# Performance work log

Measured on AMD Instinct MI355X. Metric: run time of the kernel, lower is better.

The kernel has to match this reference:

```python
import jax, jax.numpy as jnp
import numpy as np

B, N, S = 32, 1000, 200
D, H, DK, FF, NL = 128, 8, 16, 512, 3
HK = H * DK


def _mha(x, Wq, Wk, Wv, Wo, bo):
    # x: [B, L, D]; manual multi-head attention matching the torch code
    Bv, L, _ = x.shape
    q = (x @ Wq).reshape(Bv, L, H, DK).transpose(0, 2, 1, 3)  # [B,H,L,dk]
    k = (x @ Wk).reshape(Bv, L, H, DK).transpose(0, 2, 1, 3)
    v = (x @ Wv).reshape(Bv, L, H, DK).transpose(0, 2, 1, 3)
    score = jnp.einsum('bhid,bhjd->bhij', q, k) / jnp.sqrt(jnp.asarray(DK, x.dtype))
    w = jax.nn.softmax(score, axis=-1)
    o = jnp.einsum('bhij,bhjd->bhid', w, v).transpose(0, 2, 1, 3).reshape(Bv, L, HK)
    return o @ Wo + bo


def _decoder_layer(x, Wq, Wk, Wv, Wo, bo, W1, b1, W2, b2):
    out1 = x + _mha(x, Wq, Wk, Wv, Wo, bo)
    ff = jax.nn.relu(out1 @ W1 + b1) @ W2 + b2
    return out1 + ff


def _forward(data, attention_bias, Wfirst, bfirst, Wlast, blast,
             Wq, Wk, Wv, Wo, bo, W1, b1, W2, b2, Wfin, bfin, sel):
    Bv, Np, Dm = data.shape
    Sn = sel.shape[1]
    bidx = jnp.arange(Bv)
    # _get_new_data: ordered list of unselected node indices, shape [B, N-S]
    mask = jnp.zeros((Bv, Np), bool).at[bidx[:, None], sel].set(True)
    vals = jnp.where(mask, Np, jnp.arange(Np)[None, :])
    unselect = jnp.sort(vals, axis=1)[:, : Np - Sn]            # [B, N-S]
    left = jnp.take_along_axis(data, unselect[:, :, None], axis=1)  # [B, N-S, D]
    # _get_encoding for first / last selected node
    first = data[bidx, sel[:, 0]]
    last = data[bidx, sel[:, -1]]
    ef = first @ Wfirst + bfirst
    el = last @ Wlast + blast
    out = jnp.concatenate([ef[:, None], left, el[:, None]], axis=1)  # [B, N-S+2, D]
    for i in range(Wq.shape[0]):
        out = _decoder_layer(out, Wq[i], Wk[i], Wv[i], Wo[i], bo[i],
                             W1[i], b1[i], W2[i], b2[i])
    logits = (out @ Wfin + bfin)[..., 0]                       # [B, N-S+2]
    # attention bias of current (last selected) node, gathered at unselected
    ab_cur = attention_bias[bidx, sel[:, -1]]                  # [B, N]
    ab_uns = jnp.take_along_axis(ab_cur, unselect, axis=1)     # [B, N-S]
    logits = logits.at[:, 1:-1].add(ab_uns)
    L = logits.shape[1]
    pos = jnp.arange(L)
    end_mask = (pos == 0) | (pos == L - 1)
    logits = jnp.where(end_mask[None, :], -jnp.inf, logits)
    props = jax.nn.softmax(logits, axis=-1)[:, 1:-1]           # [B, N-S]
    props = jnp.where(props <= 1e-5, props + 1e-7, props)
    # scatter back: selected positions -> -2, unselected -> props
    new_props = jnp.full((Bv, Np), -2.0, dtype=data.dtype)
    new_props = new_props.at[bidx[:, None], unselect].set(props)
    return new_props


def setup_inputs() -> dict:
    key = jax.random.key(0)
    ks = jax.random.split(key, 24)
    data = jax.random.normal(ks[0], (B, N, D), jnp.float32)
    # selected_node_list must contain unique indices per row (partial tour)
    sel = jax.vmap(lambda k: jax.random.permutation(k, N))(
        jax.random.split(ks[1], B))[:, :S].astype(jnp.int32)
    attention_bias = jax.random.normal(ks[2], (B, N, N), jnp.float32)

    def lin(k, shape, fan_in):
        return jax.random.normal(k, shape, jnp.float32) / np.float32(np.sqrt(fan_in))

    return dict(
        data=data,
        attention_bias=attention_bias,
        Wfirst=lin(ks[3], (D, D), D), bfirst=jnp.zeros((D,), jnp.float32),
        Wlast=lin(ks[4], (D, D), D), blast=jnp.zeros((D,), jnp.float32),
        Wq=lin(ks[5], (NL, D, HK), D),
        Wk=lin(ks[6], (NL, D, HK), D),
        Wv=lin(ks[7], (NL, D, HK), D),
        Wo=lin(ks[8], (NL, HK, D), HK), bo=jnp.zeros((NL, D), jnp.float32),
        W1=lin(ks[9], (NL, D, FF), D), b1=jnp.zeros((NL, FF), jnp.float32),
        W2=lin(ks[10], (NL, FF, D), FF), b2=jnp.zeros((NL, D), jnp.float32),
        Wfin=lin(ks[11], (D, 1), D), bfin=jnp.zeros((1,), jnp.float32),
        selected_node_list=sel,
    )


def reference(data, attention_bias, Wfirst, bfirst, Wlast, blast,
              Wq, Wk, Wv, Wo, bo, W1, b1, W2, b2, Wfin, bfin,
              selected_node_list):
    return _forward(data, attention_bias, Wfirst, bfirst, Wlast, blast,
                    Wq, Wk, Wv, Wo, bo, W1, b1, W2, b2, Wfin, bfin,
                    selected_node_list)
```

## Files before the change

kernel.cpp:

```cpp
#include <hip/hip_runtime.h>
#include <hip/hip_bf16.h>
#include <math.h>

#define NB 32
#define NN 1000
#define SS 200
#define DD 128
#define HH 8
#define DKK 16
#define FFD 512
#define NLAYER 3
#define LQ 802
#define LPAD 832
#define NPADK (LPAD - LQ)
#define MROWS (NB*LQ)
#define NBLK64 (MROWS/64)
#define NQT 26
#define NQT64 13
#define HSTR 516
#define TSTR 132

typedef __attribute__((ext_vector_type(8))) short short8;
typedef __attribute__((ext_vector_type(4))) short short4v;
typedef __attribute__((ext_vector_type(16))) float f32x16;

static __device__ __forceinline__ unsigned short f2bf(float x) {
  union { float f; unsigned int u; } v; v.f = x;
  unsigned int r = v.u + 0x7fff + ((v.u >> 16) & 1);
  return (unsigned short)(r >> 16);
}

#define WCH 196608
__global__ __launch_bounds__(256) void k_wconv(const float* __restrict__ Wq, const float* __restrict__ Wk,
                       const float* __restrict__ Wv, const float* __restrict__ Wo,
                       const float* __restrict__ W1, const float* __restrict__ W2,
                       unsigned short* __restrict__ WtQKV, unsigned short* __restrict__ Wot,
                       unsigned short* __restrict__ W1t, unsigned short* __restrict__ W2t) {
  int e = blockIdx.x*256 + threadIdx.x;
  if (e >= 3*WCH) return;
  int layer = e / WCH, r = e - layer*WCH;
  if (r < 49152) {
    int n = r >> 7, k = r & 127;
    int sect = n >> 7, nn = n & 127;
    const float* W = (sect == 0) ? Wq : (sect == 1) ? Wk : Wv;
    WtQKV[layer*49152 + r] = f2bf(W[layer*16384 + k*128 + nn]);
  } else if (r < 65536) {
    int r2 = r - 49152;
    int n = r2 >> 7, k = r2 & 127;
    Wot[layer*16384 + r2] = f2bf(Wo[layer*16384 + k*128 + n]);
  } else if (r < 131072) {
    int r2 = r - 65536;
    int n = r2 >> 7, k = r2 & 127;
    W1t[layer*65536 + r2] = f2bf(W1[layer*65536 + k*512 + n]);
  } else {
    int r2 = r - 131072;
    int n = r2 >> 9, k = r2 & 511;
    W2t[layer*65536 + r2] = f2bf(W2[layer*65536 + k*128 + n]);
  }
}

__global__ __launch_bounds__(1024) void k_unselect(const int* __restrict__ sel,
                                                   int* __restrict__ unselect,
                                                   int* __restrict__ pos) {
  int b = blockIdx.x;
  int n = threadIdx.x;
  __shared__ int bufA[1024];
  __shared__ int bufB[1024];
  bufA[n] = (n < NN) ? 1 : 0;
  __syncthreads();
  if (n < SS) bufA[sel[b*SS + n]] = 0;
  __syncthreads();
  int flag = bufA[n];
  int* src = bufA; int* dst = bufB;
  for (int off = 1; off < 1024; off <<= 1) {
    int v = src[n];
    if (n >= off) v += src[n - off];
    __syncthreads();
    dst[n] = v;
    __syncthreads();
    int* tp = src; src = dst; dst = tp;
  }
  if (n < NN) {
    if (flag) {
      int j = src[n] - 1;
      unselect[b*800 + j] = n;
      pos[b*NN + n] = j + 1;
    } else {
      pos[b*NN + n] = -1;
    }
  }
}

__global__ __launch_bounds__(128) void k_embed_ends(const float* __restrict__ data,
                       const int* __restrict__ sel,
                       const float* __restrict__ Wfirst, const float* __restrict__ bfirst,
                       const float* __restrict__ Wlast, const float* __restrict__ blast,
                       float* __restrict__ X, unsigned short* __restrict__ Xbf) {
  int which = blockIdx.x, b = blockIdx.y, d = threadIdx.x;
  int l = (which == 0) ? 0 : LQ-1;
  __shared__ float xr[DD];
  int src = sel[b*SS + (which == 0 ? 0 : SS-1)];
  const float* W    = (which == 0) ? Wfirst : Wlast;
  const float* bias = (which == 0) ? bfirst : blast;
  xr[d] = data[((size_t)b*NN + src)*DD + d];
  __syncthreads();
  float acc = bias[d];
  #pragma unroll 4
  for (int k = 0; k < DD; ++k) acc += xr[k] * W[k*DD + d];
  size_t off = ((size_t)(b*LQ + l))*DD + d;
  X[off] = acc;
  Xbf[off] = f2bf(acc);
}

__global__ __launch_bounds__(256) void k_embed_mid(const float* __restrict__ data,
                       const int* __restrict__ unselect,
                       float* __restrict__ X, unsigned short* __restrict__ Xbf) {
  int e = blockIdx.x*256 + threadIdx.x;
  int r = e >> 5;
  int c4 = (e & 31) * 4;
  int b = r / 800, j = r - b*800;
  int nidx = unselect[r];
  const float4 v = *(const float4*)&data[((size_t)b*NN + nidx)*DD + c4];
  size_t off = ((size_t)(b*LQ + 1 + j))*DD + c4;
  *(float4*)&X[off] = v;
  unsigned short p0 = f2bf(v.x), p1 = f2bf(v.y), p2 = f2bf(v.z), p3 = f2bf(v.w);
  ushort4 pk; pk.x = p0; pk.y = p1; pk.z = p2; pk.w = p3;
  *(ushort4*)&Xbf[off] = pk;
}

__global__ __launch_bounds__(256) void k_qkv_mfma(const unsigned short* __restrict__ Xbf,
                       const unsigned short* __restrict__ Wt,
                       unsigned short* __restrict__ Qb, unsigned short* __restrict__ Kb,
                       unsigned short* __restrict__ Vb) {
  int row0 = blockIdx.x * 64;
  int t = threadIdx.x, wave = t >> 6, lane = t & 63;
  int col = lane & 31, half = lane >> 5;
  short8 a[2][8];
  const unsigned short* xb = Xbf + (size_t)(row0 + col)*DD + half*8;
  #pragma unroll
  for (int mi = 0; mi < 2; ++mi)
    #pragma unroll
    for (int s = 0; s < 8; ++s)
      a[mi][s] = *(const short8*)(xb + (size_t)mi*32*DD + s*16);
  #pragma unroll
  for (int nn = 0; nn < 3; ++nn) {
    int ni = wave*3 + nn;
    short8 bfr[8];
    const unsigned short* wb = Wt + (size_t)(ni*32 + col)*DD + half*8;
    #pragma unroll
    for (int s = 0; s < 8; ++s) bfr[s] = *(const short8*)(wb + s*16);
    f32x16 acc0 = {0.f,0.f,0.f,0.f,0.f,0.f,0.f,0.f,0.f,0.f,0.f,0.f,0.f,0.f,0.f,0.f};
    f32x16 acc1 = {0.f,0.f,0.f,0.f,0.f,0.f,0.f,0.f,0.f,0.f,0.f,0.f,0.f,0.f,0.f,0.f};
    #pragma unroll
    for (int s = 0; s < 8; ++s) {
      acc0 = __builtin_amdgcn_mfma_f32_32x32x16_bf16(a[0][s], bfr[s], acc0, 0, 0, 0);
      acc1 = __builtin_amdgcn_mfma_f32_32x32x16_bf16(a[1][s], bfr[s], acc1, 0, 0, 0);
    }
    int n = ni*32 + col;
    int sect = n >> 7, nc = n & 127;
    int h = nc >> 4, d = nc & 15;
    #pragma unroll
    for (int mi = 0; mi < 2; ++mi) {
      const f32x16& acc = mi ? acc1 : acc0;
      #pragma unroll
      for (int r = 0; r < 16; ++r) {
        int m = row0 + mi*32 + (r&3) + 8*(r>>2) + 4*half;
        int b_ = m / LQ, l = m - b_*LQ;
        size_t bh = (size_t)(b_*HH + h);
        float v = acc[r];
        if (sect == 0)      Qb[(bh*LPAD + l)*DKK + d] = f2bf(v * 0.25f);
        else if (sect == 1) Kb[(bh*LPAD + l)*DKK + d] = f2bf(v);
        else                Vb[(bh*LPAD + l)*DKK + d] = f2bf(v);
      }
    }
  }
}

__global__ __launch_bounds__(256) void k_vt(const unsigned short* __restrict__ Vb,
                                            unsigned short* __restrict__ Vt,
                                            unsigned short* __restrict__ Kb) {
  __shared__ unsigned short Lt[16][72];
  int l0 = blockIdx.x * 64;
  int bh = blockIdx.y;
  int t = threadIdx.x;
  int l = t >> 2, d4 = (t & 3) * 4;
  ushort4 v = {0,0,0,0};
  if (l0 + l < LQ) v = *(const ushort4*)&Vb[((size_t)bh*LPAD + l0 + l)*DKK + d4];
  Lt[d4+0][l] = v.x; Lt[d4+1][l] = v.y; Lt[d4+2][l] = v.z; Lt[d4+3][l] = v.w;
  __syncthreads();
  int dk = t >> 4, lq = (t & 15)*4;
  ushort4 o;
  o.x = Lt[dk][lq]; o.y = Lt[dk][lq+1]; o.z = Lt[dk][lq+2]; o.w = Lt[dk][lq+3];
  *(ushort4*)&Vt[((size_t)bh*DKK + dk)*LPAD + l0 + lq] = o;
  if (blockIdx.x == 12 && t < 240)
    ((unsigned int*)&Kb[((size_t)bh*LPAD + LQ)*DKK])[t] = 0u;
}

__global__ __launch_bounds__(256) void k_attn3(const unsigned short* __restrict__ Q,
                       const unsigned short* __restrict__ K,
                       const unsigned short* __restrict__ Vt,
                       unsigned short* __restrict__ Obf) {
  int bid = blockIdx.x;
  int g = bid & 7, i = bid >> 3;
  int bhg = i / NQT64, qt = i - bhg*NQT64;
  int bh = bhg*8 + g;
  int b = bh >> 3, h = bh & 7;
  int q0 = qt*64;
  size_t bhL = (size_t)bh * LPAD;
  int t = threadIdx.x;
  int wave = t >> 6, lane = t & 63;
  int col = lane & 31;
  int half = lane >> 5;
  bool hb = (half != 0);

  __shared__ float mw[2][4][32];
  __shared__ float sw[2][4][32];
  __shared__ float sfin[2][32];
  __shared__ float ored[2][4][16][32];
  __shared__ float osum[2][32][17];

  int q0c = q0 + col;      if (q0c > LQ-1) q0c = LQ-1;
  int q1c = q0 + 32 + col; if (q1c > LQ-1) q1c = LQ-1;
  short8 bQ0 = *(const short8*)&Q[(bhL + q0c)*DKK + half*8];
  short8 bQ1 = *(const short8*)&Q[(bhL + q1c)*DKK + half*8];

  f32x16 oacc0 = {0.f,0.f,0.f,0.f,0.f,0.f,0.f,0.f,0.f,0.f,0.f,0.f,0.f,0.f,0.f,0.f};
  f32x16 oacc1 = oacc0;
  float runm0 = -INFINITY, runs0 = 0.f;
  float runm1 = -INFINITY, runs1 = 0.f;

  for (int kt = wave; kt < NQT; kt += 4) {
    int key0 = kt*32;
    short8 aK = *(const short8*)&K[(bhL + key0 + col)*DKK + half*8];
    short8 aV0 = {0,0,0,0,0,0,0,0};
    short8 aV1 = {0,0,0,0,0,0,0,0};
    if (col < 16) {
      const unsigned short* vp = &Vt[((size_t)bh*DKK + col)*LPAD + key0 + half*8];
      aV0 = *(const short8*)vp;
      aV1 = *(const short8*)(vp + 16);
    }

    auto process = [&](const short8& bQ, f32x16& oacc, float& runm, float& runs) {
      f32x16 c = {0.f,0.f,0.f,0.f,0.f,0.f,0.f,0.f,0.f,0.f,0.f,0.f,0.f,0.f,0.f,0.f};
      c = __builtin_amdgcn_mfma_f32_32x32x16_bf16(aK, bQ, c, 0, 0, 0);
      float tm = c[0];
      #pragma unroll
      for (int r = 1; r < 16; ++r) tm = fmaxf(tm, c[r]);
      tm = fmaxf(tm, __shfl_xor(tm, 32, 64));
      float mnew = fmaxf(runm, tm);
      float scale = __expf(runm - mnew);
      runs *= scale;
      #pragma unroll
      for (int r = 0; r < 8; ++r) oacc[r] *= scale;
      runm = mnew;
      float p[16];
      #pragma unroll
      for (int r = 0; r < 16; ++r) p[r] = __expf(c[r] - mnew);
      float ts = 0.f;
      #pragma unroll
      for (int r = 0; r < 16; ++r) ts += p[r];
      runs += ts;
      unsigned int pk[8];
      #pragma unroll
      for (int j = 0; j < 8; ++j) {
        unsigned int ua = __float_as_uint(p[2*j]);
        unsigned int ub = __float_as_uint(p[2*j+1]);
        pk[j] = (ua >> 16) | (ub & 0xffff0000u);
      }
      int Y0 = __shfl_xor((int)(hb ? pk[0] : pk[2]), 32, 64);
      int Y1 = __shfl_xor((int)(hb ? pk[1] : pk[3]), 32, 64);
      int Y2 = __shfl_xor((int)(hb ? pk[4] : pk[6]), 32, 64);
      int Y3 = __shfl_xor((int)(hb ? pk[5] : pk[7]), 32, 64);
      union { int4 i4; short8 s8; } fA, fB;
      fA.i4.x = hb ? Y0 : (int)pk[0];
      fA.i4.y = hb ? Y1 : (int)pk[1];
      fA.i4.z = hb ? (int)pk[2] : Y0;
      fA.i4.w = hb ? (int)pk[3] : Y1;
      fB.i4.x = hb ? Y2 : (int)pk[4];
      fB.i4.y = hb ? Y3 : (int)pk[5];
      fB.i4.z = hb ? (int)pk[6] : Y2;
      fB.i4.w = hb ? (int)pk[7] : Y3;
      oacc = __builtin_amdgcn_mfma_f32_32x32x16_bf16(aV0, fA.s8, oacc, 0, 0, 0);
      oacc = __builtin_amdgcn_mfma_f32_32x32x16_bf16(aV1, fB.s8, oacc, 0, 0, 0);
    };
    process(bQ0, oacc0, runm0, runs0);
    process(bQ1, oacc1, runm1, runs1);
  }

  float m2v[2], fsv[2];
  #pragma unroll
  for (int u = 0; u < 2; ++u) {
    float runm = u ? runm1 : runm0;
    float runs = u ? runs1 : runs0;
    float pm = __shfl_xor(runm, 32, 64);
    float ps = __shfl_xor(runs, 32, 64);
    float m2 = fmaxf(runm, pm);
    float fself = __expf(runm - m2);
    float s2 = runs*fself + ps*__expf(pm - m2);
    if (half == 0) { mw[u][wave][col] = m2; sw[u][wave][col] = s2; }
    m2v[u] = m2; fsv[u] = fself;
  }
  __syncthreads();
  #pragma unroll
  for (int u = 0; u < 2; ++u) {
    float M = fmaxf(fmaxf(mw[u][0][col], mw[u][1][col]), fmaxf(mw[u][2][col], mw[u][3][col]));
    float S = sw[u][0][col]*__expf(mw[u][0][col]-M) + sw[u][1][col]*__expf(mw[u][1][col]-M)
            + sw[u][2][col]*__expf(mw[u][2][col]-M) + sw[u][3][col]*__expf(mw[u][3][col]-M);
    float fw = __expf(m2v[u] - M) * fsv[u];
    const f32x16& oacc = u ? oacc1 : oacc0;
    #pragma unroll
    for (int r = 0; r < 8; ++r) {
      int dv = (r&3) + 8*(r>>2) + 4*half;
      ored[u][wave][dv][col] = oacc[r] * fw;
    }
    if (wave == 0 && half == 0)
      sfin[u][col] = S - (float)NPADK * __expf(-M);
  }
  __syncthreads();
  {
    int qq = t & 31, dv0 = t >> 5;
    #pragma unroll
    for (int u = 0; u < 2; ++u)
      #pragma unroll
      for (int k = 0; k < 2; ++k) {
        int dv = dv0 + 8*k;
        osum[u][qq][dv] = ored[u][0][dv][qq] + ored[u][1][dv][qq]
                        + ored[u][2][dv][qq] + ored[u][3][dv][qq];
      }
  }
  __syncthreads();
  {
    int qs = t >> 3, c2 = (t & 7)*2;
    #pragma unroll
    for (int u = 0; u < 2; ++u) {
      int q = q0 + u*32 + qs;
      if (q < LQ) {
        float invS = 1.f / sfin[u][qs];
        unsigned int lo = f2bf(osum[u][qs][c2]   * invS);
        unsigned int hi = f2bf(osum[u][qs][c2+1] * invS);
        *(unsigned int*)&Obf[((size_t)(b*LQ + q))*DD + h*DKK + c2] = lo | (hi << 16);
      }
    }
  }
}

__global__ __launch_bounds__(256) void k_pff(const unsigned short* __restrict__ Obf,
        const unsigned short* __restrict__ Wot, const float* __restrict__ bo,
        const unsigned short* __restrict__ W1t, const float* __restrict__ b1,
        const unsigned short* __restrict__ W2t, const float* __restrict__ b2,
        float* __restrict__ X, unsigned short* __restrict__ Xbf) {
  __shared__ __align__(16) unsigned short LDSU[64 * HSTR];
  unsigned short* T  = LDSU;
  unsigned short* Hs = LDSU;
  int row0 = blockIdx.x * 64;
  int t = threadIdx.x, wave = t >> 6, lane = t & 63;
  int col = lane & 31, half = lane >> 5;
  int n = wave*32 + col;
  float res[2][16];
  {
    short8 a[2][8];
    const unsigned short* ob = Obf + (size_t)(row0 + col)*DD + half*8;
    #pragma unroll
    for (int mi = 0; mi < 2; ++mi)
      #pragma unroll
      for (int s = 0; s < 8; ++s)
        a[mi][s] = *(const short8*)(ob + (size_t)mi*32*DD + s*16);
    short8 bfr[8];
    const unsigned short* wb = Wot + (size_t)n*DD + half*8;
    #pragma unroll
    for (int s = 0; s < 8; ++s) bfr[s] = *(const short8*)(wb + s*16);
    f32x16 acc0 = {0.f,0.f,0.f,0.f,0.f,0.f,0.f,0.f,0.f,0.f,0.f,0.f,0.f,0.f,0.f,0.f};
    f32x16 acc1 = acc0;
    #pragma unroll
    for (int s = 0; s < 8; ++s) {
      acc0 = __builtin_amdgcn_mfma_f32_32x32x16_bf16(a[0][s], bfr[s], acc0, 0, 0, 0);
      acc1 = __builtin_amdgcn_mfma_f32_32x32x16_bf16(a[1][s], bfr[s], acc1, 0, 0, 0);
    }
    float bv = bo[n];
    #pragma unroll
    for (int mi = 0; mi < 2; ++mi) {
      const f32x16& acc = mi ? acc1 : acc0;
      #pragma unroll
      for (int r = 0; r < 16; ++r) {
        int ml = mi*32 + (r&3) + 8*(r>>2) + 4*half;
        size_t off = (size_t)(row0 + ml)*DD + n;
        res[mi][r] = X[off] + acc[r] + bv;
        T[ml*TSTR + n] = f2bf(res[mi][r]);
      }
    }
  }
  __syncthreads();
  short8 aF[2][8];
  #pragma unroll
  for (int mi = 0; mi < 2; ++mi)
    #pragma unroll
    for (int s = 0; s < 8; ++s) {
      const unsigned short* tp = &T[(mi*32 + col)*TSTR + half*8 + s*16];
      union { short4v h[2]; short8 v; } u;
      u.h[0] = *(const short4v*)tp;
      u.h[1] = *(const short4v*)(tp + 4);
      aF[mi][s] = u.v;
    }
  __syncthreads();
  #pragma unroll
  for (int nn = 0; nn < 4; ++nn) {
    int ni = wave*4 + nn;
    short8 bfr[8];
    const unsigned short* wb = W1t + (size_t)(ni*32 + col)*DD + half*8;
    #pragma unroll
    for (int s = 0; s < 8; ++s) bfr[s] = *(const short8*)(wb + s*16);
    f32x16 acc0 = {0.f,0.f,0.f,0.f,0.f,0.f,0.f,0.f,0.f,0.f,0.f,0.f,0.f,0.f,0.f,0.f};
    f32x16 acc1 = acc0;
    #pragma unroll
    for (int s = 0; s < 8; ++s) {
      acc0 = __builtin_amdgcn_mfma_f32_32x32x16_bf16(aF[0][s], bfr[s], acc0, 0, 0, 0);
      acc1 = __builtin_amdgcn_mfma_f32_32x32x16_bf16(aF[1][s], bfr[s], acc1, 0, 0, 0);
    }
    int nf = ni*32 + col;
    float bv = b1[nf];
    #pragma unroll
    for (int mi = 0; mi < 2; ++mi) {
      const f32x16& acc = mi ? acc1 : acc0;
      #pragma unroll
      for (int r = 0; r < 16; ++r) {
        int ml = mi*32 + (r&3) + 8*(r>>2) + 4*half;
        Hs[ml*HSTR + nf] = f2bf(fmaxf(acc[r] + bv, 0.f));
      }
    }
  }
  __syncthreads();
  f32x16 acc0 = {0.f,0.f,0.f,0.f,0.f,0.f,0.f,0.f,0.f,0.f,0.f,0.f,0.f,0.f,0.f,0.f};
  f32x16 acc1 = acc0;
  const unsigned short* w2b = W2t + (size_t)n*FFD + half*8;
  #pragma unroll 4
  for (int s = 0; s < 32; ++s) {
    int ko = s*16 + half*8;
    union { short4v h[2]; short8 v; } h0, h1;
    const unsigned short* hp0 = &Hs[col*HSTR + ko];
    const unsigned short* hp1 = &Hs[(32 + col)*HSTR + ko];
    h0.h[0] = *(const short4v*)hp0;  h0.h[1] = *(const short4v*)(hp0 + 4);
    h1.h[0] = *(const short4v*)hp1;  h1.h[1] = *(const short4v*)(hp1 + 4);
    short8 bfr = *(const short8*)(w2b + s*16);
    acc0 = __builtin_amdgcn_mfma_f32_32x32x16_bf16(h0.v, bfr, acc0, 0, 0, 0);
    acc1 = __builtin_amdgcn_mfma_f32_32x32x16_bf16(h1.v, bfr, acc1, 0, 0, 0);
  }
  float bv = b2[n];
  #pragma unroll
  for (int mi = 0; mi < 2; ++mi) {
    const f32x16& acc = mi ? acc1 : acc0;
    #pragma unroll
    for (int r = 0; r < 16; ++r) {
      int ml = mi*32 + (r&3) + 8*(r>>2) + 4*half;
      size_t off = (size_t)(row0 + ml)*DD + n;
      float v = res[mi][r] + acc[r] + bv;
      X[off] = v;
      Xbf[off] = f2bf(v);
    }
  }
}

__global__ __launch_bounds__(256) void k_logits(const float* __restrict__ X,
                        const float* __restrict__ Wfin, const float* __restrict__ bfin,
                        float* __restrict__ logits) {
  int t = threadIdx.x, wave = t >> 6, lane = t & 63;
  int row = blockIdx.x*4 + wave;
  float2 xv = *(const float2*)&X[(size_t)row*DD + lane*2];
  float2 wv = *(const float2*)&Wfin[lane*2];
  float v = xv.x*wv.x + xv.y*wv.y;
  #pragma unroll
  for (int off = 32; off > 0; off >>= 1) v += __shfl_down(v, off);
  if (lane == 0) logits[row] = v + bfin[0];
}

__global__ __launch_bounds__(256) void k_final(const float* __restrict__ logits,
                       const float* __restrict__ AB, const int* __restrict__ sel,
                       const int* __restrict__ unselect, const int* __restrict__ pos,
                       float* __restrict__ out) {
  int b = blockIdx.x, t = threadIdx.x;
  __shared__ float sl[800];
  __shared__ float red[256];
  int lastsel = sel[b*SS + SS-1];
  const float* abrow = AB + ((size_t)b*NN + lastsel)*NN;
  for (int j = t; j < 800; j += 256)
    sl[j] = logits[b*LQ + j + 1] + abrow[unselect[b*800 + j]];
  __syncthreads();
  float lm = -INFINITY;
  for (int j = t; j < 800; j += 256) lm = fmaxf(lm, sl[j]);
  red[t] = lm;
  __syncthreads();
  for (int s = 128; s > 0; s >>= 1) {
    if (t < s) red[t] = fmaxf(red[t], red[t+s]);
    __syncthreads();
  }
  float m = red[0];
  __syncthreads();
  float ls = 0.f;
  for (int j = t; j < 800; j += 256) ls += __expf(sl[j] - m);
  red[t] = ls;
  __syncthreads();
  for (int s = 128; s > 0; s >>= 1) {
    if (t < s) red[t] += red[t+s];
    __syncthreads();
  }
  float inv = 1.f / red[0];
  for (int n = t; n < NN; n += 256) {
    int p1 = pos[b*NN + n];
    float v = -2.0f;
    if (p1 >= 0) {
      float p = __expf(sl[p1-1] - m) * inv;
      if (p <= 1e-5f) p += 1e-7f;
      v = p;
    }
    out[(size_t)b*NN + n] = v;
  }
}

extern "C" void kernel_launch(void* const* d_in, const int* in_sizes, int n_in,
                              void* d_out, int out_size, void* d_ws, size_t ws_size,
                              hipStream_t stream) {
  const float* data   = (const float*)d_in[0];
  const float* AB     = (const float*)d_in[1];
  const float* Wfirst = (const float*)d_in[2];
  const float* bfirst = (const float*)d_in[3];
  const float* Wlast  = (const float*)d_in[4];
  const float* blast  = (const float*)d_in[5];
  const float* Wq     = (const float*)d_in[6];
  const float* Wk     = (const float*)d_in[7];
  const float* Wv     = (const float*)d_in[8];
  const float* Wo     = (const float*)d_in[9];
  const float* bo     = (const float*)d_in[10];
  const float* W1     = (const float*)d_in[11];
  const float* b1     = (const float*)d_in[12];
  const float* W2     = (const float*)d_in[13];
  const float* b2     = (const float*)d_in[14];
  const float* Wfin   = (const float*)d_in[15];
  const float* bfin   = (const float*)d_in[16];
  const int*   sel    = (const int*)d_in[17];
  float* out = (float*)d_out;
  (void)in_sizes; (void)n_in; (void)out_size; (void)ws_size;

  char* ws = (char*)d_ws;
  const size_t NELT = (size_t)MROWS * DD;
  const size_t KVELT = (size_t)NB*HH*LPAD*DKK;
  int*   UNSEL = (int*)ws;
  int*   POS   = (int*)(ws + 102400);
  float* X     = (float*)(ws + 230400);
  unsigned short* Xbf = (unsigned short*)(X + NELT);
  unsigned short* Ob  = Xbf + NELT;
  unsigned short* Qb  = Ob + NELT;
  unsigned short* Kb  = Qb + KVELT;
  unsigned short* Vb  = Kb + KVELT;
  unsigned short* Vt  = Vb + KVELT;
  unsigned short* WtQKV = Vt + KVELT;
  unsigned short* Wot = WtQKV + (size_t)NLAYER*384*128;
  unsigned short* W1t = Wot + (size_t)NLAYER*128*128;
  unsigned short* W2t = W1t + (size_t)NLAYER*512*128;
  float* LOG = (float*)(W2t + (size_t)NLAYER*128*512);

  k_wconv<<<(3*WCH + 255)/256, 256, 0, stream>>>(Wq, Wk, Wv, Wo, W1, W2, WtQKV, Wot, W1t, W2t);
  k_unselect<<<NB, 1024, 0, stream>>>(sel, UNSEL, POS);
  k_embed_ends<<<dim3(2, NB), 128, 0, stream>>>(data, sel, Wfirst, bfirst, Wlast, blast, X, Xbf);
  k_embed_mid<<<3200, 256, 0, stream>>>(data, UNSEL, X, Xbf);
  for (int i = 0; i < NLAYER; ++i) {
    k_qkv_mfma<<<NBLK64, 256, 0, stream>>>(Xbf, WtQKV + (size_t)i*384*128, Qb, Kb, Vb);
    k_vt<<<dim3(13, NB*HH), 256, 0, stream>>>(Vb, Vt, Kb);
    k_attn3<<<NQT64*HH*NB, 256, 0, stream>>>(Qb, Kb, Vt, Ob);
    k_pff<<<NBLK64, 256, 0, stream>>>(Ob, Wot + (size_t)i*128*128, bo + (size_t)i*DD,
                                      W1t + (size_t)i*512*128, b1 + (size_t)i*FFD,
                                      W2t + (size_t)i*128*512, b2 + (size_t)i*DD, X, Xbf);
  }
  k_logits<<<MROWS/4, 256, 0, stream>>>(X, Wfin, bfin, LOG);
  k_final<<<NB, 256, 0, stream>>>(LOG, AB, sel, UNSEL, POS, out);
}
```

Baseline: 557.3 us.

## Restructure attention to one query tile per wave with lazy rescale and exp2

The attention kernel now gives each wave its own 32-query tile and has it walk all key tiles. Before, four waves split the keys and merged partial softmax results through shared memory and several barriers. The query scale folds in log2(e) so exp2 can be used, and the running max is only updated when a tile exceeds it by a threshold. Packed bf16 conversion and max3 instructions replace manual bit tricks. Separately, the unselect prefix sum uses wave ballots instead of a log-step scan, and QKV scatter avoids per-element division; the gains trade fewer waves per block and lazy-rescale numeric risk for removed reductions.

```diff
diff --git a/kernel.cpp b/kernel.cpp
--- a/kernel.cpp
+++ b/kernel.cpp
@@ -16,9 +16,10 @@
 #define MROWS (NB*LQ)
 #define NBLK64 (MROWS/64)
 #define NQT 26
-#define NQT64 13
+#define NQB 7
 #define HSTR 516
 #define TSTR 132
+#define QSCALE 0.3606737602f
 
 typedef __attribute__((ext_vector_type(8))) short short8;
 typedef __attribute__((ext_vector_type(4))) short short4v;
@@ -28,6 +29,18 @@
   union { float f; unsigned int u; } v; v.f = x;
   unsigned int r = v.u + 0x7fff + ((v.u >> 16) & 1);
   return (unsigned short)(r >> 16);
+}
+
+static __device__ __forceinline__ unsigned int cvtpk_bf16(float lo, float hi) {
+  unsigned int r;
+  asm("v_cvt_pk_bf16_f32 %0, %1, %2" : "=v"(r) : "v"(lo), "v"(hi));
+  return r;
+}
+
+static __device__ __forceinline__ float max3f(float a, float b, float c) {
+  float r;
+  asm("v_max3_f32 %0, %1, %2, %3" : "=v"(r) : "v"(a), "v"(b), "v"(c));
+  return r;
 }
 
 #define WCH 196608
@@ -64,25 +77,24 @@
                                                    int* __restrict__ pos) {
   int b = blockIdx.x;
   int n = threadIdx.x;
-  __shared__ int bufA[1024];
-  __shared__ int bufB[1024];
-  bufA[n] = (n < NN) ? 1 : 0;
-  __syncthreads();
-  if (n < SS) bufA[sel[b*SS + n]] = 0;
-  __syncthreads();
-  int flag = bufA[n];
-  int* src = bufA; int* dst = bufB;
-  for (int off = 1; off < 1024; off <<= 1) {
-    int v = src[n];
-    if (n >= off) v += src[n - off];
-    __syncthreads();
-    dst[n] = v;
-    __syncthreads();
-    int* tp = src; src = dst; dst = tp;
-  }
+  __shared__ unsigned char fl[1024];
+  __shared__ int wsum[16];
+  fl[n] = (n < NN) ? 1 : 0;
+  __syncthreads();
+  if (n < SS) fl[sel[b*SS + n]] = 0;
+  __syncthreads();
+  int flag = fl[n];
+  unsigned long long m = __ballot(flag);
+  int lane = n & 63, w = n >> 6;
+  int pre = __popcll(m & ((1ULL << lane) - 1ULL));
+  if (lane == 63) wsum[w] = pre + flag;
+  __syncthreads();
+  int off = 0;
+  #pragma unroll
+  for (int i = 0; i < 16; ++i) off += (i < w) ? wsum[i] : 0;
   if (n < NN) {
     if (flag) {
-      int j = src[n] - 1;
+      int j = off + pre;
       unselect[b*800 + j] = n;
       pos[b*NN + n] = j + 1;
     } else {
@@ -135,6 +147,9 @@
   int row0 = blockIdx.x * 64;
   int t = threadIdx.x, wave = t >> 6, lane = t & 63;
   int col = lane & 31, half = lane >> 5;
+  int b0 = row0 / LQ;
+  int l00 = row0 - b0*LQ;
+  int split = LQ - l00;
   short8 a[2][8];
   const unsigned short* xb = Xbf + (size_t)(row0 + col)*DD + half*8;
   #pragma unroll
@@ -164,11 +179,13 @@
       const f32x16& acc = mi ? acc1 : acc0;
       #pragma unroll
       for (int r = 0; r < 16; ++r) {
-        int m = row0 + mi*32 + (r&3) + 8*(r>>2) + 4*half;
-        int b_ = m / LQ, l = m - b_*LQ;
+        int ml = mi*32 + (r&3) + 8*(r>>2) + 4*half;
+        int over = (ml >= split);
+        int b_ = b0 + over;
+        int l  = over ? (ml - split) : (l00 + ml);
         size_t bh = (size_t)(b_*HH + h);
         float v = acc[r];
-        if (sect == 0)      Qb[(bh*LPAD + l)*DKK + d] = f2bf(v * 0.25f);
+        if (sect == 0)      Qb[(bh*LPAD + l)*DKK + d] = f2bf(v * QSCALE);
         else if (sect == 1) Kb[(bh*LPAD + l)*DKK + d] = f2bf(v);
         else                Vb[(bh*LPAD + l)*DKK + d] = f2bf(v);
       }
@@ -202,34 +219,27 @@
                        unsigned short* __restrict__ Obf) {
   int bid = blockIdx.x;
   int g = bid & 7, i = bid >> 3;
-  int bhg = i / NQT64, qt = i - bhg*NQT64;
+  int bhg = i / NQB, qt = i - bhg*NQB;
   int bh = bhg*8 + g;
   int b = bh >> 3, h = bh & 7;
-  int q0 = qt*64;
   size_t bhL = (size_t)bh * LPAD;
   int t = threadIdx.x;
   int wave = t >> 6, lane = t & 63;
-  int col = lane & 31;
-  int half = lane >> 5;
+  int col = lane & 31, half = lane >> 5;
   bool hb = (half != 0);
 
-  __shared__ float mw[2][4][32];
-  __shared__ float sw[2][4][32];
-  __shared__ float sfin[2][32];
-  __shared__ float ored[2][4][16][32];
-  __shared__ float osum[2][32][17];
-
-  int q0c = q0 + col;      if (q0c > LQ-1) q0c = LQ-1;
-  int q1c = q0 + 32 + col; if (q1c > LQ-1) q1c = LQ-1;
-  short8 bQ0 = *(const short8*)&Q[(bhL + q0c)*DKK + half*8];
-  short8 bQ1 = *(const short8*)&Q[(bhL + q1c)*DKK + half*8];
-
-  f32x16 oacc0 = {0.f,0.f,0.f,0.f,0.f,0.f,0.f,0.f,0.f,0.f,0.f,0.f,0.f,0.f,0.f,0.f};
-  f32x16 oacc1 = oacc0;
-  float runm0 = -INFINITY, runs0 = 0.f;
-  float runm1 = -INFINITY, runs1 = 0.f;
-
-  for (int kt = wave; kt < NQT; kt += 4) {
+  __shared__ __align__(16) unsigned short SO[4][32][20];
+
+  int q0w = qt*128 + wave*32;
+  if (q0w >= LPAD) return;
+
+  int qc = q0w + col; if (qc > LQ-1) qc = LQ-1;
+  short8 bQ = *(const short8*)&Q[(bhL + qc)*DKK + half*8];
+
+  f32x16 oacc = {0.f,0.f,0.f,0.f,0.f,0.f,0.f,0.f,0.f,0.f,0.f,0.f,0.f,0.f,0.f,0.f};
+  float runm = -INFINITY, runs = 0.f;
+
+  for (int kt = 0; kt < NQT; ++kt) {
     int key0 = kt*32;
     short8 aK = *(const short8*)&K[(bhL + key0 + col)*DKK + half*8];
     short8 aV0 = {0,0,0,0,0,0,0,0};
@@ -239,108 +249,74 @@
       aV0 = *(const short8*)vp;
       aV1 = *(const short8*)(vp + 16);
     }
-
-    auto process = [&](const short8& bQ, f32x16& oacc, float& runm, float& runs) {
-      f32x16 c = {0.f,0.f,0.f,0.f,0.f,0.f,0.f,0.f,0.f,0.f,0.f,0.f,0.f,0.f,0.f,0.f};
-      c = __builtin_amdgcn_mfma_f32_32x32x16_bf16(aK, bQ, c, 0, 0, 0);
-      float tm = c[0];
+    f32x16 c = {0.f,0.f,0.f,0.f,0.f,0.f,0.f,0.f,0.f,0.f,0.f,0.f,0.f,0.f,0.f,0.f};
+    c = __builtin_amdgcn_mfma_f32_32x32x16_bf16(aK, bQ, c, 0, 0, 0);
+    float m0 = max3f(c[0],  c[1],  c[2]);
+    float m1 = max3f(c[3],  c[4],  c[5]);
+    float m2 = max3f(c[6],  c[7],  c[8]);
+    float m3 = max3f(c[9],  c[10], c[11]);
+    float m4 = max3f(c[12], c[13], c[14]);
+    float tm = fmaxf(max3f(m0, m1, m2), max3f(m3, m4, c[15]));
+    tm = fmaxf(tm, __shfl_xor(tm, 32, 64));
+    if (!__all(tm <= runm + 11.0f)) {
+      float mnew = fmaxf(runm, tm);
+      float sc = exp2f(runm - mnew);
+      runs *= sc;
       #pragma unroll
-      for (int r = 1; r < 16; ++r) tm = fmaxf(tm, c[r]);
-      tm = fmaxf(tm, __shfl_xor(tm, 32, 64));
-      float mnew = fmaxf(runm, tm);
-      float scale = __expf(runm - mnew);
-      runs *= scale;
-      #pragma unroll
-      for (int r = 0; r < 8; ++r) oacc[r] *= scale;
+      for (int r = 0; r < 8; ++r) oacc[r] *= sc;
       runm = mnew;
-      float p[16];
-      #pragma unroll
-      for (int r = 0; r < 16; ++r) p[r] = __expf(c[r] - mnew);
-      float ts = 0.f;
-      #pragma unroll
-      for (int r = 0; r < 16; ++r) ts += p[r];
-      runs += ts;
-      unsigned int pk[8];
-      #pragma unroll
-      for (int j = 0; j < 8; ++j) {
-        unsigned int ua = __float_as_uint(p[2*j]);
-        unsigned int ub = __float_as_uint(p[2*j+1]);
-        pk[j] = (ua >> 16) | (ub & 0xffff0000u);
-      }
-      int Y0 = __shfl_xor((int)(hb ? pk[0] : pk[2]), 32, 64);
-      int Y1 = __shfl_xor((int)(hb ? pk[1] : pk[3]), 32, 64);
-      int Y2 = __shfl_xor((int)(hb ? pk[4] : pk[6]), 32, 64);
-      int Y3 = __shfl_xor((int)(hb ? pk[5] : pk[7]), 32, 64);
-      union { int4 i4; short8 s8; } fA, fB;
-      fA.i4.x = hb ? Y0 : (int)pk[0];
-      fA.i4.y = hb ? Y1 : (int)pk[1];
-      fA.i4.z = hb ? (int)pk[2] : Y0;
-      fA.i4.w = hb ? (int)pk[3] : Y1;
-      fB.i4.x = hb ? Y2 : (int)pk[4];
-      fB.i4.y = hb ? Y3 : (int)pk[5];
-      fB.i4.z = hb ? (int)pk[6] : Y2;
-      fB.i4.w = hb ? (int)pk[7] : Y3;
-      oacc = __builtin_amdgcn_mfma_f32_32x32x16_bf16(aV0, fA.s8, oacc, 0, 0, 0);
-      oacc = __builtin_amdgcn_mfma_f32_32x32x16_bf16(aV1, fB.s8, oacc, 0, 0, 0);
-    };
-    process(bQ0, oacc0, runm0, runs0);
-    process(bQ1, oacc1, runm1, runs1);
-  }
-
-  float m2v[2], fsv[2];
-  #pragma unroll
-  for (int u = 0; u < 2; ++u) {
-    float runm = u ? runm1 : runm0;
-    float runs = u ? runs1 : runs0;
-    float pm = __shfl_xor(runm, 32, 64);
-    float ps = __shfl_xor(runs, 32, 64);
-    float m2 = fmaxf(runm, pm);
-    float fself = __expf(runm - m2);
-    float s2 = runs*fself + ps*__expf(pm - m2);
-    if (half == 0) { mw[u][wave][col] = m2; sw[u][wave][col] = s2; }
-    m2v[u] = m2; fsv[u] = fself;
-  }
-  __syncthreads();
-  #pragma unroll
-  for (int u = 0; u < 2; ++u) {
-    float M = fmaxf(fmaxf(mw[u][0][col], mw[u][1][col]), fmaxf(mw[u][2][col], mw[u][3][col]));
-    float S = sw[u][0][col]*__expf(mw[u][0][col]-M) + sw[u][1][col]*__expf(mw[u][1][col]-M)
-            + sw[u][2][col]*__expf(mw[u][2][col]-M) + sw[u][3][col]*__expf(mw[u][3][col]-M);
-    float fw = __expf(m2v[u] - M) * fsv[u];
-    const f32x16& oacc = u ? oacc1 : oacc0;
-    #pragma unroll
-    for (int r = 0; r < 8; ++r) {
-      int dv = (r&3) + 8*(r>>2) + 4*half;
-      ored[u][wave][dv][col] = oacc[r] * fw;
-    }
-    if (wave == 0 && half == 0)
-      sfin[u][col] = S - (float)NPADK * __expf(-M);
-  }
-  __syncthreads();
-  {
-    int qq = t & 31, dv0 = t >> 5;
-    #pragma unroll
-    for (int u = 0; u < 2; ++u)
-      #pragma unroll
-      for (int k = 0; k < 2; ++k) {
-        int dv = dv0 + 8*k;
-        osum[u][qq][dv] = ored[u][0][dv][qq] + ored[u][1][dv][qq]
-                        + ored[u][2][dv][qq] + ored[u][3][dv][qq];
-      }
-  }
-  __syncthreads();
-  {
-    int qs = t >> 3, c2 = (t & 7)*2;
-    #pragma unroll
-    for (int u = 0; u < 2; ++u) {
-      int q = q0 + u*32 + qs;
-      if (q < LQ) {
-        float invS = 1.f / sfin[u][qs];
-        unsigned int lo = f2bf(osum[u][qs][c2]   * invS);
-        unsigned int hi = f2bf(osum[u][qs][c2+1] * invS);
-        *(unsigned int*)&Obf[((size_t)(b*LQ + q))*DD + h*DKK + c2] = lo | (hi << 16);
-      }
-    }
+    }
+    float p[16];
+    #pragma unroll
+    for (int r = 0; r < 16; ++r) p[r] = exp2f(c[r] - runm);
+    float s01 = p[0]+p[1],  s23 = p[2]+p[3],  s45 = p[4]+p[5],   s67 = p[6]+p[7];
+    float s89 = p[8]+p[9],  sab = p[10]+p[11], scd = p[12]+p[13], sef = p[14]+p[15];
+    runs += ((s01+s23)+(s45+s67)) + ((s89+sab)+(scd+sef));
+    unsigned int pk[8];
+    #pragma unroll
+    for (int j = 0; j < 8; ++j) pk[j] = cvtpk_bf16(p[2*j], p[2*j+1]);
+    int Y0 = __shfl_xor((int)(hb ? pk[0] : pk[2]), 32, 64);
+    int Y1 = __shfl_xor((int)(hb ? pk[1] : pk[3]), 32, 64);
+    int Y2 = __shfl_xor((int)(hb ? pk[4] : pk[6]), 32, 64);
+    int Y3 = __shfl_xor((int)(hb ? pk[5] : pk[7]), 32, 64);
+    union { int4 i4; short8 s8; } fA, fB;
+    fA.i4.x = hb ? Y0 : (int)pk[0];
+    fA.i4.y = hb ? Y1 : (int)pk[1];
+    fA.i4.z = hb ? (int)pk[2] : Y0;
+    fA.i4.w = hb ? (int)pk[3] : Y1;
+    fB.i4.x = hb ? Y2 : (int)pk[4];
+    fB.i4.y = hb ? Y3 : (int)pk[5];
+    fB.i4.z = hb ? (int)pk[6] : Y2;
+    fB.i4.w = hb ? (int)pk[7] : Y3;
+    oacc = __builtin_amdgcn_mfma_f32_32x32x16_bf16(aV0, fA.s8, oacc, 0, 0, 0);
+    oacc = __builtin_amdgcn_mfma_f32_32x32x16_bf16(aV1, fB.s8, oacc, 0, 0, 0);
+  }
+
+  float pm = __shfl_xor(runm, 32, 64);
+  float ps = __shfl_xor(runs, 32, 64);
+  float M = fmaxf(runm, pm);
+  float S = runs*exp2f(runm - M) + ps*exp2f(pm - M) - (float)NPADK*exp2f(-M);
+  float invS = 1.f / S;
+
+  unsigned int o0 = cvtpk_bf16(oacc[0]*invS, oacc[1]*invS);
+  unsigned int o1 = cvtpk_bf16(oacc[2]*invS, oacc[3]*invS);
+  unsigned int o2 = cvtpk_bf16(oacc[4]*invS, oacc[5]*invS);
+  unsigned int o3 = cvtpk_bf16(oacc[6]*invS, oacc[7]*invS);
+  int dbase = 4*half;
+  *(unsigned int*)&SO[wave][col][dbase+0]  = o0;
+  *(unsigned int*)&SO[wave][col][dbase+2]  = o1;
+  *(unsigned int*)&SO[wave][col][dbase+8]  = o2;
+  *(unsigned int*)&SO[wave][col][dbase+10] = o3;
+  asm volatile("s_waitcnt lgkmcnt(0)" ::: "memory");
+  __builtin_amdgcn_sched_barrier(0);
+  #pragma unroll
+  for (int pass = 0; pass < 2; ++pass) {
+    int q = pass*16 + (lane >> 2);
+    int s = lane & 3;
+    ushort4 v = *(const ushort4*)&SO[wave][q][s*4];
+    int qq = q0w + q;
+    if (qq < LQ)
+      *(ushort4*)&Obf[((size_t)(b*LQ + qq))*DD + h*DKK + s*4] = v;
   }
 }
 
@@ -564,7 +540,7 @@
   for (int i = 0; i < NLAYER; ++i) {
     k_qkv_mfma<<<NBLK64, 256, 0, stream>>>(Xbf, WtQKV + (size_t)i*384*128, Qb, Kb, Vb);
     k_vt<<<dim3(13, NB*HH), 256, 0, stream>>>(Vb, Vt, Kb);
-    k_attn3<<<NQT64*HH*NB, 256, 0, stream>>>(Qb, Kb, Vt, Ob);
+    k_attn3<<<NQB*HH*NB, 256, 0, stream>>>(Qb, Kb, Vt, Ob);
     k_pff<<<NBLK64, 256, 0, stream>>>(Ob, Wot + (size_t)i*128*128, bo + (size_t)i*DD,
                                       W1t + (size_t)i*512*128, b1 + (size_t)i*FFD,
                                       W2t + (size_t)i*128*512, b2 + (size_t)i*DD, X, Xbf);
```

Result: slower. 587.2 us (+5.4%).

## Use base-2 softmax with lazy rescaling, hardware bf16 packing, and ballot scan

Applied to the files above, without the earlier changes.

The query scale is folded with log2(e) so the attention softmax can use raw v_exp_f32 (exp2) in place of __expf. Rescaling of the running max is skipped while the tile max stays within a threshold of the current max, and the row max now uses v_max3. Float-to-bf16 packing uses v_cvt_pk_bf16_f32 in place of truncation and shifts. Separately, the unselect prefix scan is replaced by wave ballot/popcount, and the QKV scatter avoids a per-element divide. The lazy rescale lets exponent values grow up to about 2^11 before a rescale, which trades some bf16 precision margin for fewer multiplies.

```diff
diff --git a/kernel.cpp b/kernel.cpp
--- a/kernel.cpp
+++ b/kernel.cpp
@@ -19,6 +19,7 @@
 #define NQT64 13
 #define HSTR 516
 #define TSTR 132
+#define QSCALE 0.3606737602f
 
 typedef __attribute__((ext_vector_type(8))) short short8;
 typedef __attribute__((ext_vector_type(4))) short short4v;
@@ -28,6 +29,24 @@
   union { float f; unsigned int u; } v; v.f = x;
   unsigned int r = v.u + 0x7fff + ((v.u >> 16) & 1);
   return (unsigned short)(r >> 16);
+}
+
+static __device__ __forceinline__ unsigned int cvtpk_bf16(float lo, float hi) {
+  unsigned int r;
+  asm("v_cvt_pk_bf16_f32 %0, %1, %2" : "=v"(r) : "v"(lo), "v"(hi));
+  return r;
+}
+
+static __device__ __forceinline__ float max3f(float a, float b, float c) {
+  float r;
+  asm("v_max3_f32 %0, %1, %2, %3" : "=v"(r) : "v"(a), "v"(b), "v"(c));
+  return r;
+}
+
+static __device__ __forceinline__ float exp2n(float x) {
+  float r;
+  asm("v_exp_f32 %0, %1" : "=v"(r) : "v"(x));
+  return r;
 }
 
 #define WCH 196608
@@ -64,25 +83,24 @@
                                                    int* __restrict__ pos) {
   int b = blockIdx.x;
   int n = threadIdx.x;
-  __shared__ int bufA[1024];
-  __shared__ int bufB[1024];
-  bufA[n] = (n < NN) ? 1 : 0;
-  __syncthreads();
-  if (n < SS) bufA[sel[b*SS + n]] = 0;
-  __syncthreads();
-  int flag = bufA[n];
-  int* src = bufA; int* dst = bufB;
-  for (int off = 1; off < 1024; off <<= 1) {
-    int v = src[n];
-    if (n >= off) v += src[n - off];
-    __syncthreads();
-    dst[n] = v;
-    __syncthreads();
-    int* tp = src; src = dst; dst = tp;
-  }
+  __shared__ unsigned char fl[1024];
+  __shared__ int wsum[16];
+  fl[n] = (n < NN) ? 1 : 0;
+  __syncthreads();
+  if (n < SS) fl[sel[b*SS + n]] = 0;
+  __syncthreads();
+  int flag = fl[n];
+  unsigned long long m = __ballot(flag);
+  int lane = n & 63, w = n >> 6;
+  int pre = __popcll(m & ((1ULL << lane) - 1ULL));
+  if (lane == 63) wsum[w] = pre + flag;
+  __syncthreads();
+  int off = 0;
+  #pragma unroll
+  for (int i = 0; i < 16; ++i) off += (i < w) ? wsum[i] : 0;
   if (n < NN) {
     if (flag) {
-      int j = src[n] - 1;
+      int j = off + pre;
       unselect[b*800 + j] = n;
       pos[b*NN + n] = j + 1;
     } else {
@@ -135,6 +153,9 @@
   int row0 = blockIdx.x * 64;
   int t = threadIdx.x, wave = t >> 6, lane = t & 63;
   int col = lane & 31, half = lane >> 5;
+  int b0 = row0 / LQ;
+  int l00 = row0 - b0*LQ;
+  int split = LQ - l00;
   short8 a[2][8];
   const unsigned short* xb = Xbf + (size_t)(row0 + col)*DD + half*8;
   #pragma unroll
@@ -164,11 +185,13 @@
       const f32x16& acc = mi ? acc1 : acc0;
       #pragma unroll
       for (int r = 0; r < 16; ++r) {
-        int m = row0 + mi*32 + (r&3) + 8*(r>>2) + 4*half;
-        int b_ = m / LQ, l = m - b_*LQ;
+        int ml = mi*32 + (r&3) + 8*(r>>2) + 4*half;
+        int over = (ml >= split);
+        int b_ = b0 + over;
+        int l  = over ? (ml - split) : (l00 + ml);
         size_t bh = (size_t)(b_*HH + h);
         float v = acc[r];
-        if (sect == 0)      Qb[(bh*LPAD + l)*DKK + d] = f2bf(v * 0.25f);
+        if (sect == 0)      Qb[(bh*LPAD + l)*DKK + d] = f2bf(v * QSCALE);
         else if (sect == 1) Kb[(bh*LPAD + l)*DKK + d] = f2bf(v);
         else                Vb[(bh*LPAD + l)*DKK + d] = f2bf(v);
       }
@@ -243,30 +266,30 @@
     auto process = [&](const short8& bQ, f32x16& oacc, float& runm, float& runs) {
       f32x16 c = {0.f,0.f,0.f,0.f,0.f,0.f,0.f,0.f,0.f,0.f,0.f,0.f,0.f,0.f,0.f,0.f};
       c = __builtin_amdgcn_mfma_f32_32x32x16_bf16(aK, bQ, c, 0, 0, 0);
-      float tm = c[0];
-      #pragma unroll
-      for (int r = 1; r < 16; ++r) tm = fmaxf(tm, c[r]);
+      float m0 = max3f(c[0],  c[1],  c[2]);
+      float m1 = max3f(c[3],  c[4],  c[5]);
+      float m2 = max3f(c[6],  c[7],  c[8]);
+      float m3 = max3f(c[9],  c[10], c[11]);
+      float m4 = max3f(c[12], c[13], c[14]);
+      float tm = fmaxf(max3f(m0, m1, m2), max3f(m3, m4, c[15]));
       tm = fmaxf(tm, __shfl_xor(tm, 32, 64));
-      float mnew = fmaxf(runm, tm);
-      float scale = __expf(runm - mnew);
-      runs *= scale;
-      #pragma unroll
-      for (int r = 0; r < 8; ++r) oacc[r] *= scale;
-      runm = mnew;
+      if (!__all(tm <= runm + 11.0f)) {
+        float mnew = fmaxf(runm, tm);
+        float sc = exp2n(runm - mnew);
+        runs *= sc;
+        #pragma unroll
+        for (int r = 0; r < 8; ++r) oacc[r] *= sc;
+        runm = mnew;
+      }
       float p[16];
       #pragma unroll
-      for (int r = 0; r < 16; ++r) p[r] = __expf(c[r] - mnew);
-      float ts = 0.f;
-      #pragma unroll
-      for (int r = 0; r < 16; ++r) ts += p[r];
-      runs += ts;
+      for (int r = 0; r < 16; ++r) p[r] = exp2n(c[r] - runm);
+      float s01 = p[0]+p[1],  s23 = p[2]+p[3],   s45 = p[4]+p[5],   s67 = p[6]+p[7];
+      float s89 = p[8]+p[9],  sab = p[10]+p[11], scd = p[12]+p[13], sef = p[14]+p[15];
+      runs += ((s01+s23)+(s45+s67)) + ((s89+sab)+(scd+sef));
       unsigned int pk[8];
       #pragma unroll
-      for (int j = 0; j < 8; ++j) {
-        unsigned int ua = __float_as_uint(p[2*j]);
-        unsigned int ub = __float_as_uint(p[2*j+1]);
-        pk[j] = (ua >> 16) | (ub & 0xffff0000u);
-      }
+      for (int j = 0; j < 8; ++j) pk[j] = cvtpk_bf16(p[2*j], p[2*j+1]);
       int Y0 = __shfl_xor((int)(hb ? pk[0] : pk[2]), 32, 64);
       int Y1 = __shfl_xor((int)(hb ? pk[1] : pk[3]), 32, 64);
       int Y2 = __shfl_xor((int)(hb ? pk[4] : pk[6]), 32, 64);
@@ -295,8 +318,8 @@
     float pm = __shfl_xor(runm, 32, 64);
     float ps = __shfl_xor(runs, 32, 64);
     float m2 = fmaxf(runm, pm);
-    float fself = __expf(runm - m2);
-    float s2 = runs*fself + ps*__expf(pm - m2);
+    float fself = exp2n(runm - m2);
+    float s2 = runs*fself + ps*exp2n(pm - m2);
     if (half == 0) { mw[u][wave][col] = m2; sw[u][wave][col] = s2; }
     m2v[u] = m2; fsv[u] = fself;
   }
@@ -304,9 +327,9 @@
   #pragma unroll
   for (int u = 0; u < 2; ++u) {
     float M = fmaxf(fmaxf(mw[u][0][col], mw[u][1][col]), fmaxf(mw[u][2][col], mw[u][3][col]));
-    float S = sw[u][0][col]*__expf(mw[u][0][col]-M) + sw[u][1][col]*__expf(mw[u][1][col]-M)
-            + sw[u][2][col]*__expf(mw[u][2][col]-M) + sw[u][3][col]*__expf(mw[u][3][col]-M);
-    float fw = __expf(m2v[u] - M) * fsv[u];
+    float S = sw[u][0][col]*exp2n(mw[u][0][col]-M) + sw[u][1][col]*exp2n(mw[u][1][col]-M)
+            + sw[u][2][col]*exp2n(mw[u][2][col]-M) + sw[u][3][col]*exp2n(mw[u][3][col]-M);
+    float fw = exp2n(m2v[u] - M) * fsv[u];
     const f32x16& oacc = u ? oacc1 : oacc0;
     #pragma unroll
     for (int r = 0; r < 8; ++r) {
@@ -314,7 +337,7 @@
       ored[u][wave][dv][col] = oacc[r] * fw;
     }
     if (wave == 0 && half == 0)
-      sfin[u][col] = S - (float)NPADK * __expf(-M);
+      sfin[u][col] = S - (float)NPADK * exp2n(-M);
   }
   __syncthreads();
   {
@@ -336,9 +359,8 @@
       int q = q0 + u*32 + qs;
       if (q < LQ) {
         float invS = 1.f / sfin[u][qs];
-        unsigned int lo = f2bf(osum[u][qs][c2]   * invS);
-        unsigned int hi = f2bf(osum[u][qs][c2+1] * invS);
-        *(unsigned int*)&Obf[((size_t)(b*LQ + q))*DD + h*DKK + c2] = lo | (hi << 16);
+        unsigned int pkv = cvtpk_bf16(osum[u][qs][c2] * invS, osum[u][qs][c2+1] * invS);
+        *(unsigned int*)&Obf[((size_t)(b*LQ + q))*DD + h*DKK + c2] = pkv;
       }
     }
   }
```

Measured after the change: 532.1 us. 1.05x faster.
